# Kernel tuning notes

Hardware: AMD Instinct MI355X
Metric: run time of the kernel (lower is better)

The kernel has to match this reference:

```python
import jax, jax.numpy as jnp
import numpy as np


def _dwconv(x, w, pad):
    # depthwise conv, NCHW, weight (C,1,kh,kw), feature_group_count=C
    return jax.lax.conv_general_dilated(
        x, w, window_strides=(1, 1), padding=pad,
        feature_group_count=x.shape[1],
        dimension_numbers=('NCHW', 'OIHW', 'NCHW'))


def _max_channel_relu(x):
    # assumed MaxChannelReLU: keep only the channel-max value at each (b,h,w)
    return x * (x == jnp.max(x, axis=1, keepdims=True))


def setup_inputs() -> dict:
    key = jax.random.key(0)
    ks = jax.random.split(key, 6)
    B, C, H, W = 16, 64, 128, 128
    x = jax.random.normal(ks[0], (B, C, H, W), dtype=jnp.float32)
    w_bbx = 0.1 * jax.random.normal(ks[1], (C, 1, 1, 1), dtype=jnp.float32)
    w_width = 0.1 * jax.random.normal(ks[2], (C, 1, 1, 11), dtype=jnp.float32)
    w_width_sh = 0.1 * jax.random.normal(ks[3], (C, 1, 1, 1), dtype=jnp.float32)
    w_height = 0.1 * jax.random.normal(ks[4], (C, 1, 11, 1), dtype=jnp.float32)
    w_height_sh = 0.1 * jax.random.normal(ks[5], (C, 1, 1, 1), dtype=jnp.float32)
    return {"x": x, "w_bbx": w_bbx, "w_width": w_width,
            "w_width_sh": w_width_sh, "w_height": w_height,
            "w_height_sh": w_height_sh}


def reference(x, w_bbx, w_width, w_width_sh, w_height, w_height_sh):
    B, C, H, W = x.shape
    # self.bbx: depthwise 1x1 conv == per-channel scale
    wh = x * w_bbx.reshape(1, C, 1, 1)
    # width branch: depthwise (1,11) conv pad 5, scaled by W, then shared 1x1
    w = _dwconv(wh, w_width, [(0, 0), (5, 5)]) * W
    w = w * w_width_sh.reshape(1, C, 1, 1)
    # height branch: depthwise (11,1) conv pad 5, scaled by H, then shared 1x1
    h = _dwconv(wh, w_height, [(5, 5), (0, 0)]) * H
    h = h * w_height_sh.reshape(1, C, 1, 1)
    sx = jax.nn.sigmoid(x)
    M = jnp.max(sx, axis=(-2, -1), keepdims=True) - 0.01
    score = x * (sx > M).astype(x.dtype)
    S = jnp.sum(score, axis=(-2, -1), keepdims=True)
    sn = score / S  # normalized weights, reused by all weighted reductions
    ws = jnp.sum(w * sn, axis=(-2, -1))
    hs = jnp.sum(h * sn, axis=(-2, -1))
    ps = jnp.max(sx, axis=(-2, -1))
    col = jnp.arange(W, dtype=x.dtype).reshape(1, 1, 1, W)
    row = jnp.arange(H, dtype=x.dtype).reshape(1, 1, H, 1)
    x1 = jnp.sum(col * sn, axis=(-2, -1)) - ws / 2
    y1 = jnp.sum(row * sn, axis=(-2, -1)) - hs / 2
    x2 = x1 + ws
    y2 = y1 + hs
    score_m = _max_channel_relu(score)
    w_m = _max_channel_relu(w)
    h_m = _max_channel_relu(h)
    i = jnp.broadcast_to(jnp.arange(B, dtype=x.dtype)[:, None], (B, C))
    bbox = jnp.stack([i, x1, y1, x2, y2, ps], axis=-1).reshape(-1, 6)
    return jnp.concatenate([score_m, w_m, h_m], axis=1), bbox
```

## Files before the change

kernel.cpp:

```cpp
#include <hip/hip_runtime.h>
#include <math.h>

#define BATCH 16
#define CH    64
#define HH    128
#define WW    128
#define PLANE (HH*WW)
#define OUT0  (BATCH*3*CH*PLANE)

#define LROW  144
#define LROWS 138

#define CW_OFF  7168
#define CHS_OFF 7232
#define MW_OFF  8192
#define MH_OFF  270336
#define MS_OFF  532480

__device__ __forceinline__ void conv4(const float* __restrict__ base,
                                      const float* __restrict__ wk,
                                      const float* __restrict__ hk,
                                      float cw, float chs, float T,
                                      float4& w4, float4& h4, float4& s4) {
    float4 vx;
    float hx = 0.f, hy = 0.f, hz = 0.f, hw = 0.f;
#pragma unroll
    for (int k = 0; k < 11; k++) {
        float4 v = *(const float4*)(base + k * 144 + 8);
        if (k == 5) vx = v;
        hx = fmaf(v.x, hk[k], hx);
        hy = fmaf(v.y, hk[k], hy);
        hz = fmaf(v.z, hk[k], hz);
        hw = fmaf(v.w, hk[k], hw);
    }
    float wbuf[20];
    {
        float4 a0 = *(const float4*)(base + 5 * 144 + 0);
        float4 a1 = *(const float4*)(base + 5 * 144 + 4);
        float4 a3 = *(const float4*)(base + 5 * 144 + 12);
        float4 a4 = *(const float4*)(base + 5 * 144 + 16);
        wbuf[0] = a0.x;  wbuf[1] = a0.y;  wbuf[2] = a0.z;  wbuf[3] = a0.w;
        wbuf[4] = a1.x;  wbuf[5] = a1.y;  wbuf[6] = a1.z;  wbuf[7] = a1.w;
        wbuf[8] = vx.x;  wbuf[9] = vx.y;  wbuf[10] = vx.z; wbuf[11] = vx.w;
        wbuf[12] = a3.x; wbuf[13] = a3.y; wbuf[14] = a3.z; wbuf[15] = a3.w;
        wbuf[16] = a4.x; wbuf[17] = a4.y; wbuf[18] = a4.z; wbuf[19] = a4.w;
    }
    float wo[4];
#pragma unroll
    for (int j = 0; j < 4; j++) {
        float acc = 0.f;
#pragma unroll
        for (int k = 0; k < 11; k++) acc = fmaf(wbuf[j + 3 + k], wk[k], acc);
        wo[j] = acc * cw;
    }
    w4.x = wo[0]; w4.y = wo[1]; w4.z = wo[2]; w4.w = wo[3];
    h4.x = hx * chs; h4.y = hy * chs; h4.z = hz * chs; h4.w = hw * chs;
    s4.x = (vx.x > T) ? vx.x : 0.f;
    s4.y = (vx.y > T) ? vx.y : 0.f;
    s4.z = (vx.z > T) ? vx.z : 0.f;
    s4.w = (vx.w > T) ? vx.w : 0.f;
}

__global__ __launch_bounds__(256) void k_max(const float* __restrict__ x,
                                             const float* __restrict__ w_bbx,
                                             const float* __restrict__ w_width_sh,
                                             const float* __restrict__ w_height_sh,
                                             float* __restrict__ ws) {
    int bid = blockIdx.x;
    const float4* xp = (const float4*)(x + (size_t)bid * PLANE);
    int tid = threadIdx.x;
    float m = -INFINITY;
#pragma unroll
    for (int i = 0; i < 16; i++) {
        float4 v = xp[i * 256 + tid];
        m = fmaxf(m, fmaxf(fmaxf(v.x, v.y), fmaxf(v.z, v.w)));
    }
#pragma unroll
    for (int off = 32; off; off >>= 1) m = fmaxf(m, __shfl_xor(m, off, 64));
    __shared__ float sm[4];
    int wid = tid >> 6, lane = tid & 63;
    if (lane == 0) sm[wid] = m;
    __syncthreads();
    if (tid == 0) {
        float mm = fmaxf(fmaxf(sm[0], sm[1]), fmaxf(sm[2], sm[3]));
        float ps = 1.0f / (1.0f + expf(-mm));
        float M = ps - 0.01f;
        float T = (M > 0.0f) ? logf(M / (1.0f - M)) : -INFINITY;
        ws[bid] = T;
        ws[1024 + bid] = ps;
    }
    if (bid < 64 && tid == 1) {
        float cb = w_bbx[bid];
        ws[CW_OFF + bid]  = 128.0f * w_width_sh[bid] * cb;
        ws[CHS_OFF + bid] = 128.0f * w_height_sh[bid] * cb;
    }
}

__global__ __launch_bounds__(256) void k_cmax(const float* __restrict__ x,
                                              const float* __restrict__ w_width,
                                              const float* __restrict__ w_height,
                                              float* __restrict__ ws) {
    __shared__ float4 xs4[4 * 18 * 36];
    float* xs = (float*)xs4;
    int bid = blockIdx.x;
    int b = bid >> 4;
    int r0 = (bid & 15) * 8;
    int tid = threadIdx.x;

    for (int i = tid; i < 4 * 18 * 36; i += 256)
        xs4[i] = make_float4(0.f, 0.f, 0.f, 0.f);

    int lr_o = tid >> 5;
    int c0 = (tid & 31) << 2;

    float4 mw = make_float4(-INFINITY, -INFINITY, -INFINITY, -INFINITY);
    float4 mh = mw, ms = mw;

    for (int ch0 = 0; ch0 < 64; ch0 += 4) {
        __syncthreads();
        for (int j = tid; j < 4 * 576; j += 256) {
            int i = j / 576;
            int rem = j - i * 576;
            int lr = rem >> 5;
            int c4 = rem & 31;
            int gr = r0 - 5 + lr;
            if (gr >= 0 && gr < 128) {
                float4 v = *(const float4*)(x +
                    ((size_t)((b * 64 + ch0 + i) * 128 + gr)) * 128 + c4 * 4);
                *(float4*)(xs + (i * 18 + lr) * 144 + 8 + c4 * 4) = v;
            }
        }
        __syncthreads();
#pragma unroll
        for (int i = 0; i < 4; i++) {
            int c = ch0 + i;
            float T   = ws[b * 64 + c];
            float cw  = ws[CW_OFF + c];
            float chs = ws[CHS_OFF + c];
            float wk[11], hk[11];
#pragma unroll
            for (int k = 0; k < 11; k++) {
                wk[k] = w_width[c * 11 + k];
                hk[k] = w_height[c * 11 + k];
            }
            float4 w4, h4, s4;
            conv4(xs + (i * 18 + lr_o) * 144 + c0, wk, hk, cw, chs, T, w4, h4, s4);
            mw.x = fmaxf(mw.x, w4.x); mw.y = fmaxf(mw.y, w4.y);
            mw.z = fmaxf(mw.z, w4.z); mw.w = fmaxf(mw.w, w4.w);
            mh.x = fmaxf(mh.x, h4.x); mh.y = fmaxf(mh.y, h4.y);
            mh.z = fmaxf(mh.z, h4.z); mh.w = fmaxf(mh.w, h4.w);
            ms.x = fmaxf(ms.x, s4.x); ms.y = fmaxf(ms.y, s4.y);
            ms.z = fmaxf(ms.z, s4.z); ms.w = fmaxf(ms.w, s4.w);
        }
    }
    int p = b * PLANE + (r0 + lr_o) * 128 + c0;
    *(float4*)(ws + MW_OFF + p) = mw;
    *(float4*)(ws + MH_OFF + p) = mh;
    *(float4*)(ws + MS_OFF + p) = ms;
}

__global__ __launch_bounds__(256) void k_write(
    const float* __restrict__ x,
    const float* __restrict__ w_width, const float* __restrict__ w_height,
    float* __restrict__ ws, float* __restrict__ out) {
    __shared__ float xs[LROWS * LROW];
    __shared__ float red[4 * 5];
    int bid = blockIdx.x;
    int b = bid >> 6, c = bid & 63;
    int tid = threadIdx.x;

    for (int i = tid; i < LROWS * LROW; i += 256) xs[i] = 0.0f;
    __syncthreads();
    const float* xp = x + (size_t)bid * PLANE;
#pragma unroll
    for (int i = 0; i < 16; i++) {
        int idx = i * 256 + tid;
        int p = idx * 4;
        int y = p >> 7, xc = p & 127;
        float4 v = ((const float4*)xp)[idx];
        *(float4*)&xs[(y + 5) * LROW + xc + 8] = v;
    }
    float wk[11], hk[11];
#pragma unroll
    for (int k = 0; k < 11; k++) {
        wk[k] = w_width[c * 11 + k];
        hk[k] = w_height[c * 11 + k];
    }
    float T   = ws[bid];
    float cw  = ws[CW_OFF + c];
    float chs = ws[CHS_OFF + c];
    __syncthreads();

    float S = 0.f, Sw = 0.f, Sh = 0.f, Scol = 0.f, Srow = 0.f;
    float* outS = out + (size_t)(b * 192 + c) * PLANE;
    float* outW = out + (size_t)(b * 192 + 64 + c) * PLANE;
    float* outH = out + (size_t)(b * 192 + 128 + c) * PLANE;
    const float* mwp = ws + MW_OFF + b * PLANE;
    const float* mhp = ws + MH_OFF + b * PLANE;
    const float* msp = ws + MS_OFF + b * PLANE;

    for (int g = 0; g < 16; g++) {
        int idx = g * 256 + tid;
        int p = idx * 4;
        int y = p >> 7, xc = p & 127;
        float4 w4, h4, s4;
        conv4(xs + y * LROW + xc, wk, hk, cw, chs, T, w4, h4, s4);

        float s4sum = s4.x + s4.y + s4.z + s4.w;
        S += s4sum;
        Srow += (float)y * s4sum;
        Sw = fmaf(w4.x, s4.x, Sw); Sw = fmaf(w4.y, s4.y, Sw);
        Sw = fmaf(w4.z, s4.z, Sw); Sw = fmaf(w4.w, s4.w, Sw);
        Sh = fmaf(h4.x, s4.x, Sh); Sh = fmaf(h4.y, s4.y, Sh);
        Sh = fmaf(h4.z, s4.z, Sh); Sh = fmaf(h4.w, s4.w, Sh);
        Scol = fmaf((float)(xc + 0), s4.x, Scol);
        Scol = fmaf((float)(xc + 1), s4.y, Scol);
        Scol = fmaf((float)(xc + 2), s4.z, Scol);
        Scol = fmaf((float)(xc + 3), s4.w, Scol);

        float4 mw = *(const float4*)(mwp + p);
        float4 mh = *(const float4*)(mhp + p);
        float4 ms = *(const float4*)(msp + p);
        float4 o;
        o.x = (s4.x == ms.x) ? s4.x : 0.f;
        o.y = (s4.y == ms.y) ? s4.y : 0.f;
        o.z = (s4.z == ms.z) ? s4.z : 0.f;
        o.w = (s4.w == ms.w) ? s4.w : 0.f;
        ((float4*)outS)[idx] = o;
        o.x = (w4.x == mw.x) ? w4.x : 0.f;
        o.y = (w4.y == mw.y) ? w4.y : 0.f;
        o.z = (w4.z == mw.z) ? w4.z : 0.f;
        o.w = (w4.w == mw.w) ? w4.w : 0.f;
        ((float4*)outW)[idx] = o;
        o.x = (h4.x == mh.x) ? h4.x : 0.f;
        o.y = (h4.y == mh.y) ? h4.y : 0.f;
        o.z = (h4.z == mh.z) ? h4.z : 0.f;
        o.w = (h4.w == mh.w) ? h4.w : 0.f;
        ((float4*)outH)[idx] = o;
    }
#pragma unroll
    for (int off = 32; off; off >>= 1) {
        S    += __shfl_xor(S, off, 64);
        Sw   += __shfl_xor(Sw, off, 64);
        Sh   += __shfl_xor(Sh, off, 64);
        Scol += __shfl_xor(Scol, off, 64);
        Srow += __shfl_xor(Srow, off, 64);
    }
    int wid = tid >> 6, lane = tid & 63;
    if (lane == 0) {
        red[wid * 5 + 0] = S;   red[wid * 5 + 1] = Sw;
        red[wid * 5 + 2] = Sh;  red[wid * 5 + 3] = Scol;
        red[wid * 5 + 4] = Srow;
    }
    __syncthreads();
    if (tid == 0) {
        float a0 = 0, a1 = 0, a2 = 0, a3 = 0, a4 = 0;
#pragma unroll
        for (int w2 = 0; w2 < 4; w2++) {
            a0 += red[w2 * 5 + 0]; a1 += red[w2 * 5 + 1];
            a2 += red[w2 * 5 + 2]; a3 += red[w2 * 5 + 3];
            a4 += red[w2 * 5 + 4];
        }
        ws[2048 + bid] = a0;
        ws[3072 + bid] = a1;
        ws[4096 + bid] = a2;
        ws[5120 + bid] = a3;
        ws[6144 + bid] = a4;
    }
}

__global__ __launch_bounds__(256) void k_bbox(const float* __restrict__ ws,
                                              float* __restrict__ out) {
    int idx = blockIdx.x * 256 + threadIdx.x;
    if (idx >= 1024) return;
    int b = idx >> 6;
    float S    = ws[2048 + idx];
    float Sw   = ws[3072 + idx];
    float Sh   = ws[4096 + idx];
    float Scol = ws[5120 + idx];
    float Srow = ws[6144 + idx];
    float ps   = ws[1024 + idx];
    float inv = 1.0f / S;
    float wsv = Sw * inv, hsv = Sh * inv;
    float x1 = Scol * inv - 0.5f * wsv;
    float y1 = Srow * inv - 0.5f * hsv;
    float* o = out + OUT0 + (size_t)idx * 6;
    o[0] = (float)b;
    o[1] = x1;
    o[2] = y1;
    o[3] = x1 + wsv;
    o[4] = y1 + hsv;
    o[5] = ps;
}

extern "C" void kernel_launch(void* const* d_in, const int* in_sizes, int n_in,
                              void* d_out, int out_size, void* d_ws, size_t ws_size,
                              hipStream_t stream) {
    const float* x          = (const float*)d_in[0];
    const float* w_bbx      = (const float*)d_in[1];
    const float* w_width    = (const float*)d_in[2];
    const float* w_width_sh = (const float*)d_in[3];
    const float* w_height   = (const float*)d_in[4];
    const float* w_height_sh= (const float*)d_in[5];
    float* out = (float*)d_out;
    float* ws  = (float*)d_ws;

    k_max<<<dim3(1024), dim3(256), 0, stream>>>(x, w_bbx, w_width_sh, w_height_sh, ws);
    k_cmax<<<dim3(256), dim3(256), 0, stream>>>(x, w_width, w_height, ws);
    k_write<<<dim3(1024), dim3(256), 0, stream>>>(x, w_width, w_height, ws, out);
    k_bbox<<<dim3(4), dim3(256), 0, stream>>>(ws, out);
}
```

Baseline: 356.2 us.

## Split channel-max over channel groups and halve k_write planes for more blocks

The channel-max kernel now splits the 64 channels into four groups, so it launches 1024 blocks instead of 256. A new combine kernel max-reduces the four partial maps. k_write now processes half a plane per block, giving 2048 blocks and a smaller shared-memory tile, and writes two sets of partial sums that k_bbox adds together. The goal is to fill the GPU better on the previously undersubscribed k_cmax and to raise occupancy in k_write. The cost is an extra kernel launch, extra workspace traffic for the partial maps, and some duplicated halo loads.

Measured after the change: 318.1 us. 1.12x faster.

```diff
diff --git a/kernel.cpp b/kernel.cpp
--- a/kernel.cpp
+++ b/kernel.cpp
@@ -7,15 +7,15 @@
 #define WW    128
 #define PLANE (HH*WW)
 #define OUT0  (BATCH*3*CH*PLANE)
-
-#define LROW  144
-#define LROWS 138
-
-#define CW_OFF  7168
-#define CHS_OFF 7232
-#define MW_OFF  8192
-#define MH_OFF  270336
-#define MS_OFF  532480
+#define BP    (BATCH*PLANE)
+
+#define T_OFF   0
+#define PS_OFF  1024
+#define SUM_OFF 2048
+#define CW_OFF  12288
+#define CHS_OFF 12352
+#define MAP_OFF 16384
+#define FMAP_OFF 3163136
 
 __device__ __forceinline__ void conv4(const float* __restrict__ base,
                                       const float* __restrict__ wk,
@@ -86,8 +86,8 @@
         float ps = 1.0f / (1.0f + expf(-mm));
         float M = ps - 0.01f;
         float T = (M > 0.0f) ? logf(M / (1.0f - M)) : -INFINITY;
-        ws[bid] = T;
-        ws[1024 + bid] = ps;
+        ws[T_OFF + bid] = T;
+        ws[PS_OFF + bid] = ps;
     }
     if (bid < 64 && tid == 1) {
         float cb = w_bbx[bid];
@@ -103,8 +103,10 @@
     __shared__ float4 xs4[4 * 18 * 36];
     float* xs = (float*)xs4;
     int bid = blockIdx.x;
-    int b = bid >> 4;
-    int r0 = (bid & 15) * 8;
+    int cg   = bid & 3;
+    int band = (bid >> 2) & 15;
+    int b    = bid >> 6;
+    int r0 = band * 8;
     int tid = threadIdx.x;
 
     for (int i = tid; i < 4 * 18 * 36; i += 256)
@@ -116,7 +118,8 @@
     float4 mw = make_float4(-INFINITY, -INFINITY, -INFINITY, -INFINITY);
     float4 mh = mw, ms = mw;
 
-    for (int ch0 = 0; ch0 < 64; ch0 += 4) {
+    for (int chunk = 0; chunk < 4; chunk++) {
+        int ch0 = cg * 16 + chunk * 4;
         __syncthreads();
         for (int j = tid; j < 4 * 576; j += 256) {
             int i = j / 576;
@@ -134,7 +137,7 @@
 #pragma unroll
         for (int i = 0; i < 4; i++) {
             int c = ch0 + i;
-            float T   = ws[b * 64 + c];
+            float T   = ws[T_OFF + b * 64 + c];
             float cw  = ws[CW_OFF + c];
             float chs = ws[CHS_OFF + c];
             float wk[11], hk[11];
@@ -154,31 +157,48 @@
         }
     }
     int p = b * PLANE + (r0 + lr_o) * 128 + c0;
-    *(float4*)(ws + MW_OFF + p) = mw;
-    *(float4*)(ws + MH_OFF + p) = mh;
-    *(float4*)(ws + MS_OFF + p) = ms;
+    *(float4*)(ws + MAP_OFF + (size_t)(cg * 3 + 0) * BP + p) = mw;
+    *(float4*)(ws + MAP_OFF + (size_t)(cg * 3 + 1) * BP + p) = mh;
+    *(float4*)(ws + MAP_OFF + (size_t)(cg * 3 + 2) * BP + p) = ms;
+}
+
+__global__ __launch_bounds__(256) void k_combine(float* __restrict__ ws) {
+    int id = blockIdx.x * 256 + threadIdx.x;
+    int f = id >> 16;
+    int r = id & 65535;
+    float4 m = *(const float4*)(ws + MAP_OFF + (size_t)f * BP + (size_t)r * 4);
+#pragma unroll
+    for (int g = 1; g < 4; g++) {
+        float4 v = *(const float4*)(ws + MAP_OFF + (size_t)(g * 3 + f) * BP + (size_t)r * 4);
+        m.x = fmaxf(m.x, v.x); m.y = fmaxf(m.y, v.y);
+        m.z = fmaxf(m.z, v.z); m.w = fmaxf(m.w, v.w);
+    }
+    *(float4*)(ws + FMAP_OFF + (size_t)f * BP + (size_t)r * 4) = m;
 }
 
 __global__ __launch_bounds__(256) void k_write(
     const float* __restrict__ x,
     const float* __restrict__ w_width, const float* __restrict__ w_height,
     float* __restrict__ ws, float* __restrict__ out) {
-    __shared__ float xs[LROWS * LROW];
+    __shared__ float xs[74 * 144];
     __shared__ float red[4 * 5];
     int bid = blockIdx.x;
-    int b = bid >> 6, c = bid & 63;
+    int half = bid & 1;
+    int plane = bid >> 1;
+    int b = plane >> 6, c = plane & 63;
+    int r0 = half * 64;
     int tid = threadIdx.x;
 
-    for (int i = tid; i < LROWS * LROW; i += 256) xs[i] = 0.0f;
+    float4* xs4 = (float4*)xs;
+    for (int i = tid; i < 74 * 36; i += 256) xs4[i] = make_float4(0.f, 0.f, 0.f, 0.f);
     __syncthreads();
-    const float* xp = x + (size_t)bid * PLANE;
-#pragma unroll
-    for (int i = 0; i < 16; i++) {
-        int idx = i * 256 + tid;
-        int p = idx * 4;
-        int y = p >> 7, xc = p & 127;
-        float4 v = ((const float4*)xp)[idx];
-        *(float4*)&xs[(y + 5) * LROW + xc + 8] = v;
+    const float* xp = x + (size_t)plane * PLANE;
+    for (int j = tid; j < 74 * 32; j += 256) {
+        int br = j >> 5, c4 = j & 31;
+        int gr = r0 - 5 + br;
+        if (gr >= 0 && gr < 128)
+            *(float4*)&xs[br * 144 + 8 + c4 * 4] =
+                *(const float4*)(xp + gr * 128 + c4 * 4);
     }
     float wk[11], hk[11];
 #pragma unroll
@@ -186,29 +206,29 @@
         wk[k] = w_width[c * 11 + k];
         hk[k] = w_height[c * 11 + k];
     }
-    float T   = ws[bid];
+    float T   = ws[T_OFF + plane];
     float cw  = ws[CW_OFF + c];
     float chs = ws[CHS_OFF + c];
     __syncthreads();
 
     float S = 0.f, Sw = 0.f, Sh = 0.f, Scol = 0.f, Srow = 0.f;
-    float* outS = out + (size_t)(b * 192 + c) * PLANE;
-    float* outW = out + (size_t)(b * 192 + 64 + c) * PLANE;
-    float* outH = out + (size_t)(b * 192 + 128 + c) * PLANE;
-    const float* mwp = ws + MW_OFF + b * PLANE;
-    const float* mhp = ws + MH_OFF + b * PLANE;
-    const float* msp = ws + MS_OFF + b * PLANE;
-
-    for (int g = 0; g < 16; g++) {
+    float* outS = out + (size_t)(b * 192 + c) * PLANE + r0 * 128;
+    float* outW = out + (size_t)(b * 192 + 64 + c) * PLANE + r0 * 128;
+    float* outH = out + (size_t)(b * 192 + 128 + c) * PLANE + r0 * 128;
+    const float* mwp = ws + FMAP_OFF + 0 * (size_t)BP + b * PLANE + r0 * 128;
+    const float* mhp = ws + FMAP_OFF + 1 * (size_t)BP + b * PLANE + r0 * 128;
+    const float* msp = ws + FMAP_OFF + 2 * (size_t)BP + b * PLANE + r0 * 128;
+
+    for (int g = 0; g < 8; g++) {
         int idx = g * 256 + tid;
         int p = idx * 4;
         int y = p >> 7, xc = p & 127;
         float4 w4, h4, s4;
-        conv4(xs + y * LROW + xc, wk, hk, cw, chs, T, w4, h4, s4);
+        conv4(xs + y * 144 + xc, wk, hk, cw, chs, T, w4, h4, s4);
 
         float s4sum = s4.x + s4.y + s4.z + s4.w;
         S += s4sum;
-        Srow += (float)y * s4sum;
+        Srow += (float)(r0 + y) * s4sum;
         Sw = fmaf(w4.x, s4.x, Sw); Sw = fmaf(w4.y, s4.y, Sw);
         Sw = fmaf(w4.z, s4.z, Sw); Sw = fmaf(w4.w, s4.w, Sw);
         Sh = fmaf(h4.x, s4.x, Sh); Sh = fmaf(h4.y, s4.y, Sh);
@@ -261,11 +281,12 @@
             a2 += red[w2 * 5 + 2]; a3 += red[w2 * 5 + 3];
             a4 += red[w2 * 5 + 4];
         }
-        ws[2048 + bid] = a0;
-        ws[3072 + bid] = a1;
-        ws[4096 + bid] = a2;
-        ws[5120 + bid] = a3;
-        ws[6144 + bid] = a4;
+        int base = SUM_OFF + half * 5120;
+        ws[base + 0 * 1024 + plane] = a0;
+        ws[base + 1 * 1024 + plane] = a1;
+        ws[base + 2 * 1024 + plane] = a2;
+        ws[base + 3 * 1024 + plane] = a3;
+        ws[base + 4 * 1024 + plane] = a4;
     }
 }
 
@@ -274,12 +295,12 @@
     int idx = blockIdx.x * 256 + threadIdx.x;
     if (idx >= 1024) return;
     int b = idx >> 6;
-    float S    = ws[2048 + idx];
-    float Sw   = ws[3072 + idx];
-    float Sh   = ws[4096 + idx];
-    float Scol = ws[5120 + idx];
-    float Srow = ws[6144 + idx];
-    float ps   = ws[1024 + idx];
+    float S    = ws[SUM_OFF + 0 * 1024 + idx] + ws[SUM_OFF + 5120 + 0 * 1024 + idx];
+    float Sw   = ws[SUM_OFF + 1 * 1024 + idx] + ws[SUM_OFF + 5120 + 1 * 1024 + idx];
+    float Sh   = ws[SUM_OFF + 2 * 1024 + idx] + ws[SUM_OFF + 5120 + 2 * 1024 + idx];
+    float Scol = ws[SUM_OFF + 3 * 1024 + idx] + ws[SUM_OFF + 5120 + 3 * 1024 + idx];
+    float Srow = ws[SUM_OFF + 4 * 1024 + idx] + ws[SUM_OFF + 5120 + 4 * 1024 + idx];
+    float ps   = ws[PS_OFF + idx];
     float inv = 1.0f / S;
     float wsv = Sw * inv, hsv = Sh * inv;
     float x1 = Scol * inv - 0.5f * wsv;
@@ -306,7 +327,8 @@
     float* ws  = (float*)d_ws;
 
     k_max<<<dim3(1024), dim3(256), 0, stream>>>(x, w_bbx, w_width_sh, w_height_sh, ws);
-    k_cmax<<<dim3(256), dim3(256), 0, stream>>>(x, w_width, w_height, ws);
-    k_write<<<dim3(1024), dim3(256), 0, stream>>>(x, w_width, w_height, ws, out);
+    k_cmax<<<dim3(1024), dim3(256), 0, stream>>>(x, w_width, w_height, ws);
+    k_combine<<<dim3(768), dim3(256), 0, stream>>>(ws);
+    k_write<<<dim3(2048), dim3(256), 0, stream>>>(x, w_width, w_height, ws, out);
     k_bbox<<<dim3(4), dim3(256), 0, stream>>>(ws, out);
 }
```
